# Kernel tuning notes

Hardware: AMD Instinct MI355X
Metric: run time of the kernel (lower is better)

Reference implementation:

```python
import jax, jax.numpy as jnp
import numpy as np

XDIM = 64
N = 1_000_000


def setup_inputs() -> dict:
    key = jax.random.key(0)
    k_noise, k_a, k_q, k_q0, k_x0 = jax.random.split(key, 5)
    norm_samp = jax.random.normal(k_noise, (N, XDIM), dtype=jnp.float32)
    eye = jnp.eye(XDIM, dtype=jnp.float32)
    # A: stable dynamics (default in module is 0.5*I); add small perturbation
    A = 0.5 * eye + 0.02 * jax.random.normal(k_a, (XDIM, XDIM), dtype=jnp.float32)
    # Cholesky-like innovation roots: near-identity lower-ish matrices, scaled small
    QChol = 0.1 * eye + 0.01 * jax.random.normal(k_q, (XDIM, XDIM), dtype=jnp.float32)
    Q0Chol = 0.1 * eye + 0.01 * jax.random.normal(k_q0, (XDIM, XDIM), dtype=jnp.float32)
    x0 = jax.random.normal(k_x0, (XDIM,), dtype=jnp.float32)
    return {"norm_samp": norm_samp, "A": A, "QChol": QChol, "Q0Chol": Q0Chol, "x0": x0}


def reference(norm_samp, A, QChol, Q0Chol, x0):
    """LDS.sampleX: x[0] = x0 + eps0 @ Q0Chol.T; x[t] = x[t-1] @ A.T + eps_t @ QChol.T."""
    x_init = x0 + norm_samp[0] @ Q0Chol.T            # [n]
    drive = norm_samp[1:] @ QChol.T                  # [N-1, n], batched GEMM up front

    def step(x, b):
        x_new = x @ A.T + b
        return x_new, x_new

    _, xs = jax.lax.scan(step, x_init, drive)        # [N-1, n]
    return jnp.concatenate([x_init[None, :], xs], axis=0)  # [N, n]
```

## Files before the change

kernel.cpp:

```cpp
#include <hip/hip_runtime.h>


using bf16x8 = __attribute__((ext_vector_type(8))) short;
using s16x4  = __attribute__((ext_vector_type(4))) short;
using f32x4  = __attribute__((ext_vector_type(4))) float;

#define N_STEPS   1000000
#define XD        64
#define T_CHUNK   50
#define WARM      30
#define STOT      (WARM + T_CHUNK)
#define BATCH     8
#define NB        (STOT / BATCH)
#define N_CHUNKS  (N_STEPS / T_CHUNK)
#define N_BLOCKS  (N_CHUNKS / 16)
#define CS        (BATCH * XD + 8)
#define PAD       72

__device__ __forceinline__ short f2bf(float f) {
    unsigned u = __builtin_bit_cast(unsigned, f);
    u += 0x7FFFu + ((u >> 16) & 1u);
    return (short)(u >> 16);
}
__device__ __forceinline__ float bf2f(short s) {
    return __builtin_bit_cast(float, ((unsigned)(unsigned short)s) << 16);
}

__global__ __launch_bounds__(64, 1) void lds_scan_kernel(
    const float* __restrict__ eps,
    const float* __restrict__ A,
    const float* __restrict__ Q,
    const float* __restrict__ Q0,
    const float* __restrict__ x0,
    float* __restrict__ out)
{
    __shared__ short Eb[16 * CS];
    __shared__ short Xh[16 * PAD];
    __shared__ short Xl[16 * PAD];
    __shared__ float corr[XD];
    __shared__ float e0s[XD];

    const int lane = threadIdx.x;
    const int cl   = lane & 15;
    const int g    = lane >> 4;

    for (int i = lane; i < 16 * PAD; i += 64) { Xh[i] = 0; Xl[i] = 0; }

    if (blockIdx.x == 0) e0s[lane] = eps[lane];
    __syncthreads();
    if (blockIdx.x == 0) {
        float c = x0[lane];
        #pragma unroll 8
        for (int j = 0; j < XD; ++j)
            c += (Q0[lane * XD + j] - Q[lane * XD + j]) * e0s[j];
        corr[lane] = c;
    }
    __syncthreads();

    bf16x8 Af[4][2], Qf[4][2];
    #pragma unroll
    for (int mt = 0; mt < 4; ++mt) {
        #pragma unroll
        for (int ks = 0; ks < 2; ++ks) {
            const float* ap = A + (mt * 16 + cl) * XD + ks * 32 + g * 8;
            const float* qp = Q + (mt * 16 + cl) * XD + ks * 32 + g * 8;
            bf16x8 af, qf;
            #pragma unroll
            for (int j = 0; j < 8; ++j) { af[j] = f2bf(ap[j]); qf[j] = f2bf(qp[j]); }
            Af[mt][ks] = af; Qf[mt][ks] = qf;
        }
    }

    const long chunk  = (long)blockIdx.x * 16 + cl;
    float* po = out + chunk * ((long)T_CHUNK * XD);

    f32x4 R[32];

    #define STAGE_LOAD(b)                                                          \
        _Pragma("unroll")                                                          \
        for (int c = 0; c < 16; ++c) {                                             \
            const long tb = ((long)blockIdx.x * 16 + c) * T_CHUNK - WARM + (long)(b) * BATCH; \
            _Pragma("unroll")                                                      \
            for (int h2 = 0; h2 < 2; ++h2) {                                       \
                const long trow = tb + h2 * 4 + g;            \
                if (trow >= 0)                                                     \
                    R[c * 2 + h2] = *(const f32x4*)(eps + trow * XD + cl * 4);     \
                else                                                               \
                    R[c * 2 + h2] = (f32x4){0.f, 0.f, 0.f, 0.f};                   \
            }                                                                      \
        }

    #define STAGE_WRITE()                                                          \
        _Pragma("unroll")                                                          \
        for (int c = 0; c < 16; ++c) {                                             \
            _Pragma("unroll")                                                      \
            for (int h2 = 0; h2 < 2; ++h2) {                                       \
                const f32x4 v = R[c * 2 + h2];                                     \
                s16x4 w;                                                           \
                _Pragma("unroll")                                                  \
                for (int j = 0; j < 4; ++j) w[j] = f2bf(v[j]);                     \
                const int k = h2 * 4 + g;                   \
                *(s16x4*)&Eb[c * CS + k * XD + cl * 4] = w;                        \
            }                                                                      \
        }

    STAGE_LOAD(0);
    STAGE_WRITE();

    for (int b = 0; b < NB; ++b) {
        if (b + 1 < NB) { STAGE_LOAD(b + 1); }

        #pragma unroll
        for (int k = 0; k < BATCH; ++k) {
            const int s = b * BATCH + k;

            bf16x8 ef0 = *(const bf16x8*)&Eb[cl * CS + k * XD +  0 + g * 8];
            bf16x8 ef1 = *(const bf16x8*)&Eb[cl * CS + k * XD + 32 + g * 8];

            bf16x8 xh0 = *(const bf16x8*)&Xh[cl * PAD +  0 + g * 8];
            bf16x8 xh1 = *(const bf16x8*)&Xh[cl * PAD + 32 + g * 8];
            bf16x8 xl0 = *(const bf16x8*)&Xl[cl * PAD +  0 + g * 8];
            bf16x8 xl1 = *(const bf16x8*)&Xl[cl * PAD + 32 + g * 8];

            f32x4 acc[4];
            #pragma unroll
            for (int mt = 0; mt < 4; ++mt) {
                f32x4 a  = {0.f, 0.f, 0.f, 0.f};
                f32x4 a2 = {0.f, 0.f, 0.f, 0.f};
                a  = __builtin_amdgcn_mfma_f32_16x16x32_bf16(Qf[mt][0], ef0, a,  0, 0, 0);
                a2 = __builtin_amdgcn_mfma_f32_16x16x32_bf16(Qf[mt][1], ef1, a2, 0, 0, 0);
                a  = __builtin_amdgcn_mfma_f32_16x16x32_bf16(Af[mt][0], xh0, a,  0, 0, 0);
                a2 = __builtin_amdgcn_mfma_f32_16x16x32_bf16(Af[mt][1], xh1, a2, 0, 0, 0);
                a  = __builtin_amdgcn_mfma_f32_16x16x32_bf16(Af[mt][0], xl0, a,  0, 0, 0);
                a2 = __builtin_amdgcn_mfma_f32_16x16x32_bf16(Af[mt][1], xl1, a2, 0, 0, 0);
                acc[mt] = a + a2;
            }

            if (blockIdx.x == 0 && s == WARM && cl == 0) {
                #pragma unroll
                for (int mt = 0; mt < 4; ++mt)
                    #pragma unroll
                    for (int r = 0; r < 4; ++r)
                        acc[mt][r] += corr[mt * 16 + g * 4 + r];
            }

            #pragma unroll
            for (int mt = 0; mt < 4; ++mt) {
                s16x4 hi, lo;
                #pragma unroll
                for (int r = 0; r < 4; ++r) {
                    const float v = acc[mt][r];
                    const short h = (short)(__builtin_bit_cast(unsigned, v) >> 16);
                    hi[r] = h;
                    const float rem = v - bf2f(h);
                    lo[r] = (short)(__builtin_bit_cast(unsigned, rem) >> 16);
                }
                *(s16x4*)&Xh[cl * PAD + mt * 16 + g * 4] = hi;
                *(s16x4*)&Xl[cl * PAD + mt * 16 + g * 4] = lo;
            }

            if (s >= WARM) {
                float* op = po + (long)(s - WARM) * XD;
                #pragma unroll
                for (int mt = 0; mt < 4; ++mt)
                    *(f32x4*)(op + mt * 16 + g * 4) = acc[mt];
            }
        }

        if (b + 1 < NB) { STAGE_WRITE(); }
    }
}

extern "C" void kernel_launch(void* const* d_in, const int* in_sizes, int n_in,
                              void* d_out, int out_size, void* d_ws, size_t ws_size,
                              hipStream_t stream) {
    const float* eps = (const float*)d_in[0];
    const float* A   = (const float*)d_in[1];
    const float* Q   = (const float*)d_in[2];
    const float* Q0  = (const float*)d_in[3];
    const float* x0  = (const float*)d_in[4];
    float* out = (float*)d_out;

    lds_scan_kernel<<<N_BLOCKS, 64, 0, stream>>>(eps, A, Q, Q0, x0, out);
}
```

Baseline: 498.4 us.

## Stream noise rows into LDS via async global_load_lds double buffering

```diff
diff --git a/kernel.cpp b/kernel.cpp
--- a/kernel.cpp
+++ b/kernel.cpp
@@ -1,4 +1,5 @@
 #include <hip/hip_runtime.h>
+#include <hip/hip_bf16.h>
 
 
 using bf16x8 = __attribute__((ext_vector_type(8))) short;
@@ -10,20 +11,26 @@
 #define T_CHUNK   50
 #define WARM      30
 #define STOT      (WARM + T_CHUNK)
-#define BATCH     8
+#define BATCH     4
 #define NB        (STOT / BATCH)
 #define N_CHUNKS  (N_STEPS / T_CHUNK)
 #define N_BLOCKS  (N_CHUNKS / 16)
-#define CS        (BATCH * XD + 8)
+#define CPAD      (BATCH * XD + 4)
 #define PAD       72
 
-__device__ __forceinline__ short f2bf(float f) {
+typedef const __attribute__((address_space(1))) void* as1cv;
+typedef __attribute__((address_space(3))) void*       as3v;
+
+__device__ __forceinline__ short f2bf_rne(float f) {
     unsigned u = __builtin_bit_cast(unsigned, f);
     u += 0x7FFFu + ((u >> 16) & 1u);
     return (short)(u >> 16);
 }
 __device__ __forceinline__ float bf2f(short s) {
     return __builtin_bit_cast(float, ((unsigned)(unsigned short)s) << 16);
+}
+__device__ __forceinline__ short f2bf_hw(float f) {
+    return __builtin_bit_cast(short, __float2bfloat16(f));
 }
 
 __global__ __launch_bounds__(64, 1) void lds_scan_kernel(
@@ -34,7 +41,7 @@
     const float* __restrict__ x0,
     float* __restrict__ out)
 {
-    __shared__ short Eb[16 * CS];
+    __shared__ float Eb32[2 * 16 * CPAD];
     __shared__ short Xh[16 * PAD];
     __shared__ short Xl[16 * PAD];
     __shared__ float corr[XD];
@@ -66,108 +73,132 @@
             const float* qp = Q + (mt * 16 + cl) * XD + ks * 32 + g * 8;
             bf16x8 af, qf;
             #pragma unroll
-            for (int j = 0; j < 8; ++j) { af[j] = f2bf(ap[j]); qf[j] = f2bf(qp[j]); }
+            for (int j = 0; j < 8; ++j) { af[j] = f2bf_rne(ap[j]); qf[j] = f2bf_rne(qp[j]); }
             Af[mt][ks] = af; Qf[mt][ks] = qf;
         }
     }
 
-    const long chunk  = (long)blockIdx.x * 16 + cl;
+    const long chunk = (long)blockIdx.x * 16 + cl;
     float* po = out + chunk * ((long)T_CHUNK * XD);
 
-    f32x4 R[32];
-
-    #define STAGE_LOAD(b)                                                          \
-        _Pragma("unroll")                                                          \
-        for (int c = 0; c < 16; ++c) {                                             \
-            const long tb = ((long)blockIdx.x * 16 + c) * T_CHUNK - WARM + (long)(b) * BATCH; \
-            _Pragma("unroll")                                                      \
-            for (int h2 = 0; h2 < 2; ++h2) {                                       \
-                const long trow = tb + h2 * 4 + g;            \
-                if (trow >= 0)                                                     \
-                    R[c * 2 + h2] = *(const f32x4*)(eps + trow * XD + cl * 4);     \
-                else                                                               \
-                    R[c * 2 + h2] = (f32x4){0.f, 0.f, 0.f, 0.f};                   \
-            }                                                                      \
-        }
-
-    #define STAGE_WRITE()                                                          \
-        _Pragma("unroll")                                                          \
-        for (int c = 0; c < 16; ++c) {                                             \
-            _Pragma("unroll")                                                      \
-            for (int h2 = 0; h2 < 2; ++h2) {                                       \
-                const f32x4 v = R[c * 2 + h2];                                     \
-                s16x4 w;                                                           \
-                _Pragma("unroll")                                                  \
-                for (int j = 0; j < 4; ++j) w[j] = f2bf(v[j]);                     \
-                const int k = h2 * 4 + g;                   \
-                *(s16x4*)&Eb[c * CS + k * XD + cl * 4] = w;                        \
-            }                                                                      \
-        }
-
-    STAGE_LOAD(0);
-    STAGE_WRITE();
-
-    for (int b = 0; b < NB; ++b) {
-        if (b + 1 < NB) { STAGE_LOAD(b + 1); }
-
-        #pragma unroll
-        for (int k = 0; k < BATCH; ++k) {
-            const int s = b * BATCH + k;
-
-            bf16x8 ef0 = *(const bf16x8*)&Eb[cl * CS + k * XD +  0 + g * 8];
-            bf16x8 ef1 = *(const bf16x8*)&Eb[cl * CS + k * XD + 32 + g * 8];
-
-            bf16x8 xh0 = *(const bf16x8*)&Xh[cl * PAD +  0 + g * 8];
-            bf16x8 xh1 = *(const bf16x8*)&Xh[cl * PAD + 32 + g * 8];
-            bf16x8 xl0 = *(const bf16x8*)&Xl[cl * PAD +  0 + g * 8];
-            bf16x8 xl1 = *(const bf16x8*)&Xl[cl * PAD + 32 + g * 8];
-
-            f32x4 acc[4];
-            #pragma unroll
-            for (int mt = 0; mt < 4; ++mt) {
-                f32x4 a  = {0.f, 0.f, 0.f, 0.f};
-                f32x4 a2 = {0.f, 0.f, 0.f, 0.f};
-                a  = __builtin_amdgcn_mfma_f32_16x16x32_bf16(Qf[mt][0], ef0, a,  0, 0, 0);
-                a2 = __builtin_amdgcn_mfma_f32_16x16x32_bf16(Qf[mt][1], ef1, a2, 0, 0, 0);
-                a  = __builtin_amdgcn_mfma_f32_16x16x32_bf16(Af[mt][0], xh0, a,  0, 0, 0);
-                a2 = __builtin_amdgcn_mfma_f32_16x16x32_bf16(Af[mt][1], xh1, a2, 0, 0, 0);
-                a  = __builtin_amdgcn_mfma_f32_16x16x32_bf16(Af[mt][0], xl0, a,  0, 0, 0);
-                a2 = __builtin_amdgcn_mfma_f32_16x16x32_bf16(Af[mt][1], xl1, a2, 0, 0, 0);
-                acc[mt] = a + a2;
+    auto dma_stage = [&](int b) {
+        float* lbase = &Eb32[(b & 1) * (16 * CPAD)];
+        #pragma unroll
+        for (int c = 0; c < 16; ++c) {
+            const long tb = ((long)blockIdx.x * 16 + c) * T_CHUNK - WARM + (long)b * BATCH;
+            float* lp = lbase + c * CPAD;
+            if (tb >= 0) {
+                const float* gp = eps + (tb + g) * XD + cl * 4;
+                __builtin_amdgcn_global_load_lds((as1cv)gp, (as3v)lp, 16, 0, 0);
+            } else {
+                const long trow = tb + g;
+                const long row  = trow < 0 ? 0 : trow;
+                f32x4 v = *(const f32x4*)(eps + row * XD + cl * 4);
+                if (trow < 0) v = (f32x4){0.f, 0.f, 0.f, 0.f};
+                *(f32x4*)(lp + lane * 4) = v;
             }
-
-            if (blockIdx.x == 0 && s == WARM && cl == 0) {
+        }
+    };
+
+    auto step = [&](const float* ebase, int k, int s) {
+        const float* ep = ebase + cl * CPAD + k * XD;
+        const f32x4 e0a = *(const f32x4*)(ep + g * 8);
+        const f32x4 e0b = *(const f32x4*)(ep + g * 8 + 4);
+        const f32x4 e1a = *(const f32x4*)(ep + 32 + g * 8);
+        const f32x4 e1b = *(const f32x4*)(ep + 32 + g * 8 + 4);
+        bf16x8 ef0, ef1;
+        #pragma unroll
+        for (int j = 0; j < 4; ++j) {
+            ef0[j]     = f2bf_hw(e0a[j]);
+            ef0[4 + j] = f2bf_hw(e0b[j]);
+            ef1[j]     = f2bf_hw(e1a[j]);
+            ef1[4 + j] = f2bf_hw(e1b[j]);
+        }
+
+        bf16x8 xh0 = *(const bf16x8*)&Xh[cl * PAD +  0 + g * 8];
+        bf16x8 xh1 = *(const bf16x8*)&Xh[cl * PAD + 32 + g * 8];
+        bf16x8 xl0 = *(const bf16x8*)&Xl[cl * PAD +  0 + g * 8];
+        bf16x8 xl1 = *(const bf16x8*)&Xl[cl * PAD + 32 + g * 8];
+
+        f32x4 acc[4];
+        #pragma unroll
+        for (int mt = 0; mt < 4; ++mt) {
+            f32x4 a  = {0.f, 0.f, 0.f, 0.f};
+            f32x4 a2 = {0.f, 0.f, 0.f, 0.f};
+            a  = __builtin_amdgcn_mfma_f32_16x16x32_bf16(Qf[mt][0], ef0, a,  0, 0, 0);
+            a2 = __builtin_amdgcn_mfma_f32_16x16x32_bf16(Qf[mt][1], ef1, a2, 0, 0, 0);
+            a  = __builtin_amdgcn_mfma_f32_16x16x32_bf16(Af[mt][0], xh0, a,  0, 0, 0);
+            a2 = __builtin_amdgcn_mfma_f32_16x16x32_bf16(Af[mt][1], xh1, a2, 0, 0, 0);
+            a  = __builtin_amdgcn_mfma_f32_16x16x32_bf16(Af[mt][0], xl0, a,  0, 0, 0);
+            a2 = __builtin_amdgcn_mfma_f32_16x16x32_bf16(Af[mt][1], xl1, a2, 0, 0, 0);
+            acc[mt] = a + a2;
+        }
+
+        if (blockIdx.x == 0 && s == WARM && cl == 0) {
+            #pragma unroll
+            for (int mt = 0; mt < 4; ++mt)
                 #pragma unroll
-                for (int mt = 0; mt < 4; ++mt)
-                    #pragma unroll
-                    for (int r = 0; r < 4; ++r)
-                        acc[mt][r] += corr[mt * 16 + g * 4 + r];
+                for (int r = 0; r < 4; ++r)
+                    acc[mt][r] += corr[mt * 16 + g * 4 + r];
+        }
+
+        #pragma unroll
+        for (int mt = 0; mt < 4; ++mt) {
+            s16x4 hi, lo;
+            #pragma unroll
+            for (int r = 0; r < 4; ++r) {
+                const float v = acc[mt][r];
+                const short h = (short)(__builtin_bit_cast(unsigned, v) >> 16);
+                hi[r] = h;
+                const float rem = v - bf2f(h);
+                lo[r] = (short)(__builtin_bit_cast(unsigned, rem) >> 16);
             }
-
-            #pragma unroll
-            for (int mt = 0; mt < 4; ++mt) {
-                s16x4 hi, lo;
-                #pragma unroll
-                for (int r = 0; r < 4; ++r) {
-                    const float v = acc[mt][r];
-                    const short h = (short)(__builtin_bit_cast(unsigned, v) >> 16);
-                    hi[r] = h;
-                    const float rem = v - bf2f(h);
-                    lo[r] = (short)(__builtin_bit_cast(unsigned, rem) >> 16);
-                }
-                *(s16x4*)&Xh[cl * PAD + mt * 16 + g * 4] = hi;
-                *(s16x4*)&Xl[cl * PAD + mt * 16 + g * 4] = lo;
-            }
-
-            if (s >= WARM) {
-                float* op = po + (long)(s - WARM) * XD;
-                #pragma unroll
-                for (int mt = 0; mt < 4; ++mt)
-                    *(f32x4*)(op + mt * 16 + g * 4) = acc[mt];
-            }
-        }
-
-        if (b + 1 < NB) { STAGE_WRITE(); }
+            *(s16x4*)&Xh[cl * PAD + mt * 16 + g * 4] = hi;
+            *(s16x4*)&Xl[cl * PAD + mt * 16 + g * 4] = lo;
+        }
+
+        if (s >= WARM) {
+            float* op = po + (long)(s - WARM) * XD;
+            #pragma unroll
+            for (int mt = 0; mt < 4; ++mt)
+                *(f32x4*)(op + mt * 16 + g * 4) = acc[mt];
+        }
+    };
+
+    auto run_batch = [&](int b) {
+        const float* ebase = &Eb32[(b & 1) * (16 * CPAD)];
+        #pragma unroll
+        for (int k = 0; k < BATCH; ++k) step(ebase, k, b * BATCH + k);
+    };
+
+    dma_stage(0);
+    dma_stage(1);
+
+    for (int b = 0; b < 8; ++b) {
+        asm volatile("s_waitcnt vmcnt(16)" ::: "memory");
+        run_batch(b);
+        __builtin_amdgcn_sched_barrier(0);
+        dma_stage(b + 2);
+    }
+    {
+        asm volatile("s_waitcnt vmcnt(24)" ::: "memory");
+        run_batch(8);
+        __builtin_amdgcn_sched_barrier(0);
+        dma_stage(10);
+    }
+    for (int b = 9; b < 18; ++b) {
+        asm volatile("s_waitcnt vmcnt(32)" ::: "memory");
+        run_batch(b);
+        __builtin_amdgcn_sched_barrier(0);
+        dma_stage(b + 2);
+    }
+    {
+        asm volatile("s_waitcnt vmcnt(32)" ::: "memory");
+        run_batch(18);
+    }
+    {
+        asm volatile("s_waitcnt vmcnt(16)" ::: "memory");
+        run_batch(19);
     }
 }
 
```

Measured after the change: 1.014 ms. 103% more time.

## Load noise directly into MFMA fragment registers, drop LDS eps staging

Applied to the files above, without the earlier changes.

```diff
diff --git a/kernel.cpp b/kernel.cpp
--- a/kernel.cpp
+++ b/kernel.cpp
@@ -1,4 +1,5 @@
 #include <hip/hip_runtime.h>
+#include <hip/hip_bf16.h>
 
 
 using bf16x8 = __attribute__((ext_vector_type(8))) short;
@@ -10,20 +11,22 @@
 #define T_CHUNK   50
 #define WARM      30
 #define STOT      (WARM + T_CHUNK)
-#define BATCH     8
-#define NB        (STOT / BATCH)
+#define NBATCH    (STOT / 2)
+#define WBATCH    (WARM / 2)
 #define N_CHUNKS  (N_STEPS / T_CHUNK)
 #define N_BLOCKS  (N_CHUNKS / 16)
-#define CS        (BATCH * XD + 8)
-#define PAD       72
+#define PAD       66
 
-__device__ __forceinline__ short f2bf(float f) {
+__device__ __forceinline__ short f2bf_rne(float f) {
     unsigned u = __builtin_bit_cast(unsigned, f);
     u += 0x7FFFu + ((u >> 16) & 1u);
     return (short)(u >> 16);
 }
 __device__ __forceinline__ float bf2f(short s) {
     return __builtin_bit_cast(float, ((unsigned)(unsigned short)s) << 16);
+}
+__device__ __forceinline__ short f2bf_hw(float f) {
+    return __builtin_bit_cast(short, __float2bfloat16(f));
 }
 
 __global__ __launch_bounds__(64, 1) void lds_scan_kernel(
@@ -34,7 +37,6 @@
     const float* __restrict__ x0,
     float* __restrict__ out)
 {
-    __shared__ short Eb[16 * CS];
     __shared__ short Xh[16 * PAD];
     __shared__ short Xl[16 * PAD];
     __shared__ float corr[XD];
@@ -66,108 +68,116 @@
             const float* qp = Q + (mt * 16 + cl) * XD + ks * 32 + g * 8;
             bf16x8 af, qf;
             #pragma unroll
-            for (int j = 0; j < 8; ++j) { af[j] = f2bf(ap[j]); qf[j] = f2bf(qp[j]); }
+            for (int j = 0; j < 8; ++j) { af[j] = f2bf_rne(ap[j]); qf[j] = f2bf_rne(qp[j]); }
             Af[mt][ks] = af; Qf[mt][ks] = qf;
         }
     }
 
-    const long chunk  = (long)blockIdx.x * 16 + cl;
-    float* po = out + chunk * ((long)T_CHUNK * XD);
+    const int chunk = blockIdx.x * 16 + cl;
+    const int tb    = chunk * T_CHUNK - WARM;
+    float* po = out + (long)chunk * T_CHUNK * XD;
 
-    f32x4 R[32];
+    f32x4 E[2][4];
 
-    #define STAGE_LOAD(b)                                                          \
-        _Pragma("unroll")                                                          \
-        for (int c = 0; c < 16; ++c) {                                             \
-            const long tb = ((long)blockIdx.x * 16 + c) * T_CHUNK - WARM + (long)(b) * BATCH; \
-            _Pragma("unroll")                                                      \
-            for (int h2 = 0; h2 < 2; ++h2) {                                       \
-                const long trow = tb + h2 * 4 + g;            \
-                if (trow >= 0)                                                     \
-                    R[c * 2 + h2] = *(const f32x4*)(eps + trow * XD + cl * 4);     \
-                else                                                               \
-                    R[c * 2 + h2] = (f32x4){0.f, 0.f, 0.f, 0.f};                   \
-            }                                                                      \
+    auto load_pair = [&](int b) {
+        #pragma unroll
+        for (int k = 0; k < 2; ++k) {
+            const int t  = tb + 2 * b + k;
+            const int tc = t < 0 ? 0 : t;
+            const float* p = eps + (long)tc * XD + g * 8;
+            E[k][0] = *(const f32x4*)(p);
+            E[k][1] = *(const f32x4*)(p + 4);
+            E[k][2] = *(const f32x4*)(p + 32);
+            E[k][3] = *(const f32x4*)(p + 36);
+        }
+    };
+
+    auto convert = [&](int k, bool maskable, int s, bf16x8& ef0, bf16x8& ef1) {
+        const bool z = maskable && ((tb + s) < 0);
+        #pragma unroll
+        for (int j = 0; j < 4; ++j) {
+            const float v0 = z ? 0.f : E[k][0][j];
+            const float v1 = z ? 0.f : E[k][1][j];
+            const float v2 = z ? 0.f : E[k][2][j];
+            const float v3 = z ? 0.f : E[k][3][j];
+            ef0[j]     = f2bf_hw(v0);
+            ef0[4 + j] = f2bf_hw(v1);
+            ef1[j]     = f2bf_hw(v2);
+            ef1[4 + j] = f2bf_hw(v3);
+        }
+    };
+
+    auto step = [&](bf16x8 ef0, bf16x8 ef1, int s, bool store_out, bool inject) {
+        bf16x8 xh0 = *(const bf16x8*)&Xh[cl * PAD +  0 + g * 8];
+        bf16x8 xh1 = *(const bf16x8*)&Xh[cl * PAD + 32 + g * 8];
+        bf16x8 xl0 = *(const bf16x8*)&Xl[cl * PAD +  0 + g * 8];
+        bf16x8 xl1 = *(const bf16x8*)&Xl[cl * PAD + 32 + g * 8];
+
+        f32x4 acc[4];
+        #pragma unroll
+        for (int mt = 0; mt < 4; ++mt) {
+            f32x4 a  = {0.f, 0.f, 0.f, 0.f};
+            f32x4 a2 = {0.f, 0.f, 0.f, 0.f};
+            a  = __builtin_amdgcn_mfma_f32_16x16x32_bf16(Qf[mt][0], ef0, a,  0, 0, 0);
+            a2 = __builtin_amdgcn_mfma_f32_16x16x32_bf16(Qf[mt][1], ef1, a2, 0, 0, 0);
+            a  = __builtin_amdgcn_mfma_f32_16x16x32_bf16(Af[mt][0], xh0, a,  0, 0, 0);
+            a2 = __builtin_amdgcn_mfma_f32_16x16x32_bf16(Af[mt][1], xh1, a2, 0, 0, 0);
+            a  = __builtin_amdgcn_mfma_f32_16x16x32_bf16(Af[mt][0], xl0, a,  0, 0, 0);
+            a2 = __builtin_amdgcn_mfma_f32_16x16x32_bf16(Af[mt][1], xl1, a2, 0, 0, 0);
+            acc[mt] = a + a2;
         }
 
-    #define STAGE_WRITE()                                                          \
-        _Pragma("unroll")                                                          \
-        for (int c = 0; c < 16; ++c) {                                             \
-            _Pragma("unroll")                                                      \
-            for (int h2 = 0; h2 < 2; ++h2) {                                       \
-                const f32x4 v = R[c * 2 + h2];                                     \
-                s16x4 w;                                                           \
-                _Pragma("unroll")                                                  \
-                for (int j = 0; j < 4; ++j) w[j] = f2bf(v[j]);                     \
-                const int k = h2 * 4 + g;                   \
-                *(s16x4*)&Eb[c * CS + k * XD + cl * 4] = w;                        \
-            }                                                                      \
+        if (inject && blockIdx.x == 0 && cl == 0) {
+            #pragma unroll
+            for (int mt = 0; mt < 4; ++mt)
+                #pragma unroll
+                for (int r = 0; r < 4; ++r)
+                    acc[mt][r] += corr[mt * 16 + g * 4 + r];
         }
 
-    STAGE_LOAD(0);
-    STAGE_WRITE();
-
-    for (int b = 0; b < NB; ++b) {
-        if (b + 1 < NB) { STAGE_LOAD(b + 1); }
-
         #pragma unroll
-        for (int k = 0; k < BATCH; ++k) {
-            const int s = b * BATCH + k;
-
-            bf16x8 ef0 = *(const bf16x8*)&Eb[cl * CS + k * XD +  0 + g * 8];
-            bf16x8 ef1 = *(const bf16x8*)&Eb[cl * CS + k * XD + 32 + g * 8];
-
-            bf16x8 xh0 = *(const bf16x8*)&Xh[cl * PAD +  0 + g * 8];
-            bf16x8 xh1 = *(const bf16x8*)&Xh[cl * PAD + 32 + g * 8];
-            bf16x8 xl0 = *(const bf16x8*)&Xl[cl * PAD +  0 + g * 8];
-            bf16x8 xl1 = *(const bf16x8*)&Xl[cl * PAD + 32 + g * 8];
-
-            f32x4 acc[4];
+        for (int mt = 0; mt < 4; ++mt) {
+            s16x4 hi, lo;
             #pragma unroll
-            for (int mt = 0; mt < 4; ++mt) {
-                f32x4 a  = {0.f, 0.f, 0.f, 0.f};
-                f32x4 a2 = {0.f, 0.f, 0.f, 0.f};
-                a  = __builtin_amdgcn_mfma_f32_16x16x32_bf16(Qf[mt][0], ef0, a,  0, 0, 0);
-                a2 = __builtin_amdgcn_mfma_f32_16x16x32_bf16(Qf[mt][1], ef1, a2, 0, 0, 0);
-                a  = __builtin_amdgcn_mfma_f32_16x16x32_bf16(Af[mt][0], xh0, a,  0, 0, 0);
-                a2 = __builtin_amdgcn_mfma_f32_16x16x32_bf16(Af[mt][1], xh1, a2, 0, 0, 0);
-                a  = __builtin_amdgcn_mfma_f32_16x16x32_bf16(Af[mt][0], xl0, a,  0, 0, 0);
-                a2 = __builtin_amdgcn_mfma_f32_16x16x32_bf16(Af[mt][1], xl1, a2, 0, 0, 0);
-                acc[mt] = a + a2;
+            for (int r = 0; r < 4; ++r) {
+                const float v = acc[mt][r];
+                const short h = (short)(__builtin_bit_cast(unsigned, v) >> 16);
+                hi[r] = h;
+                const float rem = v - bf2f(h);
+                lo[r] = (short)(__builtin_bit_cast(unsigned, rem) >> 16);
             }
-
-            if (blockIdx.x == 0 && s == WARM && cl == 0) {
-                #pragma unroll
-                for (int mt = 0; mt < 4; ++mt)
-                    #pragma unroll
-                    for (int r = 0; r < 4; ++r)
-                        acc[mt][r] += corr[mt * 16 + g * 4 + r];
-            }
-
-            #pragma unroll
-            for (int mt = 0; mt < 4; ++mt) {
-                s16x4 hi, lo;
-                #pragma unroll
-                for (int r = 0; r < 4; ++r) {
-                    const float v = acc[mt][r];
-                    const short h = (short)(__builtin_bit_cast(unsigned, v) >> 16);
-                    hi[r] = h;
-                    const float rem = v - bf2f(h);
-                    lo[r] = (short)(__builtin_bit_cast(unsigned, rem) >> 16);
-                }
-                *(s16x4*)&Xh[cl * PAD + mt * 16 + g * 4] = hi;
-                *(s16x4*)&Xl[cl * PAD + mt * 16 + g * 4] = lo;
-            }
-
-            if (s >= WARM) {
-                float* op = po + (long)(s - WARM) * XD;
-                #pragma unroll
-                for (int mt = 0; mt < 4; ++mt)
-                    *(f32x4*)(op + mt * 16 + g * 4) = acc[mt];
-            }
+            *(s16x4*)&Xh[cl * PAD + mt * 16 + g * 4] = hi;
+            *(s16x4*)&Xl[cl * PAD + mt * 16 + g * 4] = lo;
         }
 
-        if (b + 1 < NB) { STAGE_WRITE(); }
+        if (store_out) {
+            float* op = po + (long)(s - WARM) * XD;
+            #pragma unroll
+            for (int mt = 0; mt < 4; ++mt)
+                *(f32x4*)(op + mt * 16 + g * 4) = acc[mt];
+        }
+    };
+
+    load_pair(0);
+    asm volatile("" ::: "memory");
+
+    for (int b = 0; b < WBATCH; ++b) {
+        bf16x8 e00, e01, e10, e11;
+        convert(0, true, 2 * b,     e00, e01);
+        convert(1, true, 2 * b + 1, e10, e11);
+        load_pair(b + 1);
+        asm volatile("" ::: "memory");
+        step(e00, e01, 2 * b,     false, false);
+        step(e10, e11, 2 * b + 1, false, false);
+    }
+    for (int b = WBATCH; b < NBATCH; ++b) {
+        bf16x8 e00, e01, e10, e11;
+        convert(0, false, 2 * b,     e00, e01);
+        convert(1, false, 2 * b + 1, e10, e11);
+        if (b + 1 < NBATCH) load_pair(b + 1);
+        asm volatile("" ::: "memory");
+        step(e00, e01, 2 * b,     true, b == WBATCH);
+        step(e10, e11, 2 * b + 1, true, false);
     }
 }
 
```

Result: faster. 484.2 us (-2.9%).
